# Performance work log

Measured on AMD Instinct MI355X. Metric: run time of the kernel, lower is better.

## Reference

```python
import jax, jax.numpy as jnp
import numpy as np

N, E, IN, H, ED = 50000, 800000, 128, 128, 3
EPS = 1e-5

def _gat_conv(x, src, dst, ea, W, a_src, a_dst, We, a_edge, bias):
    n = x.shape[0]
    # add self loops; self-loop edge_attr = per-feature mean (PyG fill_value='mean')
    loops = jnp.arange(n, dtype=src.dtype)
    s = jnp.concatenate([src, loops])
    d = jnp.concatenate([dst, loops])
    ea_full = jnp.concatenate([ea, jnp.broadcast_to(ea.mean(0), (n, ea.shape[1]))], 0)
    h = x @ W                       # [n, H]
    al_s = h @ a_src                # [n]
    al_d = h @ a_dst
    al_e = (ea_full @ We) @ a_edge  # [E+n]
    alpha = jax.nn.leaky_relu(al_s[s] + al_d[d] + al_e, 0.2)
    # segment softmax over destination nodes (every node has a self loop)
    amax = jax.ops.segment_max(alpha, d, num_segments=n)
    ex = jnp.exp(alpha - amax[d])
    denom = jax.ops.segment_sum(ex, d, num_segments=n)
    coef = ex / (denom[d] + 1e-16)
    out = jax.ops.segment_sum(h[s] * coef[:, None], d, num_segments=n)
    return out + bias

def _bn(x, gamma, beta):
    mu = x.mean(0)
    var = ((x - mu) ** 2).mean(0)
    return (x - mu) * jax.lax.rsqrt(var + EPS) * gamma + beta

def setup_inputs():
    key = jax.random.key(0)
    ks = jax.random.split(key, 40)
    inp = {
        "x": jax.random.normal(ks[0], (N, IN), jnp.float32),
        "edge_index": jax.random.randint(ks[1], (2, E), 0, N, dtype=jnp.int32),
        "batch": jnp.zeros((N,), jnp.int32),
        "edge_attr": jax.random.normal(ks[2], (E, ED), jnp.float32),
    }
    i = 3
    for l, cin in ((1, IN), (2, H), (3, H)):
        s = 1.0 / np.sqrt(cin)
        inp[f"W{l}"] = jax.random.normal(ks[i], (cin, H), jnp.float32) * s; i += 1
        inp[f"as{l}"] = jax.random.normal(ks[i], (H,), jnp.float32) * 0.1; i += 1
        inp[f"ad{l}"] = jax.random.normal(ks[i], (H,), jnp.float32) * 0.1; i += 1
        inp[f"We{l}"] = jax.random.normal(ks[i], (ED, H), jnp.float32) * 0.5; i += 1
        inp[f"ae{l}"] = jax.random.normal(ks[i], (H,), jnp.float32) * 0.1; i += 1
        inp[f"b{l}"] = jnp.zeros((H,), jnp.float32)
        inp[f"g{l}"] = jnp.ones((H,), jnp.float32)
        inp[f"be{l}"] = jnp.zeros((H,), jnp.float32)
    return inp

def reference(x, edge_index, batch, edge_attr,
              W1, as1, ad1, We1, ae1, b1, g1, be1,
              W2, as2, ad2, We2, ae2, b2, g2, be2,
              W3, as3, ad3, We3, ae3, b3, g3, be3):
    src, dst = edge_index[0], edge_index[1]
    h = _gat_conv(x, src, dst, edge_attr, W1, as1, ad1, We1, ae1, b1)
    h = _bn(jax.nn.leaky_relu(h, 0.01), g1, be1)
    h = _gat_conv(h, src, dst, edge_attr, W2, as2, ad2, We2, ae2, b2)
    h = _bn(jax.nn.leaky_relu(h, 0.01), g2, be2)
    h = _gat_conv(h, src, dst, edge_attr, W3, as3, ad3, We3, ae3, b3)
    h = _bn(jax.nn.leaky_relu(h, 0.01), g3, be3)
    return h
```

## Files before the change

### kernel.cpp

```cpp
#include <hip/hip_runtime.h>
#include <math.h>


struct __align__(16) Edge { int src; float e0, e1, e2; };

__global__ void k_hist(const int* __restrict__ dst, int E, int* __restrict__ deg) {
  int i = blockIdx.x * blockDim.x + threadIdx.x;
  if (i < E) atomicAdd(&deg[dst[i]], 1);
}

__global__ void k_ea_sum(const float* __restrict__ ea, int E, float* __restrict__ ea_sum) {
  float s0 = 0.f, s1 = 0.f, s2 = 0.f;
  for (int i = blockIdx.x * blockDim.x + threadIdx.x; i < E; i += gridDim.x * blockDim.x) {
    s0 += ea[i * 3 + 0]; s1 += ea[i * 3 + 1]; s2 += ea[i * 3 + 2];
  }
  for (int off = 32; off; off >>= 1) {
    s0 += __shfl_down(s0, off); s1 += __shfl_down(s1, off); s2 += __shfl_down(s2, off);
  }
  __shared__ float ls[3][4];
  int lane = threadIdx.x & 63, w = threadIdx.x >> 6;
  if (lane == 0) { ls[0][w] = s0; ls[1][w] = s1; ls[2][w] = s2; }
  __syncthreads();
  if (threadIdx.x == 0) {
    float t0 = 0.f, t1 = 0.f, t2 = 0.f;
    for (int ww = 0; ww < 4; ++ww) { t0 += ls[0][ww]; t1 += ls[1][ww]; t2 += ls[2][ww]; }
    atomicAdd(&ea_sum[0], t0); atomicAdd(&ea_sum[1], t1); atomicAdd(&ea_sum[2], t2);
  }
}

__device__ __forceinline__ int wave_incl_scan(int x, int lane) {
  for (int off = 1; off < 64; off <<= 1) {
    int t = __shfl_up(x, off);
    if (lane >= off) x += t;
  }
  return x;
}

__global__ __launch_bounds__(1024) void k_scan_a(const int* __restrict__ deg, int n,
                                                 int* __restrict__ start,
                                                 int* __restrict__ bsum) {
  __shared__ int wsum[16];
  int t = threadIdx.x, lane = t & 63, w = t >> 6;
  int i = blockIdx.x * 1024 + t;
  int v = (i < n) ? deg[i] : 0;
  int x = wave_incl_scan(v, lane);
  if (lane == 63) wsum[w] = x;
  __syncthreads();
  if (w == 0 && lane < 16) {
    int s = wsum[lane];
    for (int off = 1; off < 16; off <<= 1) {
      int u = __shfl_up(s, off);
      if (lane >= off) s += u;
    }
    wsum[lane] = s;
  }
  __syncthreads();
  int woff = w ? wsum[w - 1] : 0;
  if (i < n) start[i] = x - v + woff;
  if (t == 1023) bsum[blockIdx.x] = wsum[15];
}

__global__ void k_scan_b(int* __restrict__ bsum, int nb, int* __restrict__ start, int n) {
  int lane = threadIdx.x;
  int v = (lane < nb) ? bsum[lane] : 0;
  int x = wave_incl_scan(v, lane);
  if (lane < nb) bsum[lane] = x - v;
  if (lane == nb - 1) start[n] = x;
}

__global__ void k_scan_c(int* __restrict__ start, const int* __restrict__ bsum, int n,
                         int* __restrict__ cursor) {
  int i = blockIdx.x * blockDim.x + threadIdx.x;
  if (i < n) {
    int s = start[i] + bsum[i >> 10];
    start[i] = s;
    cursor[i] = s;
  }
}

__global__ void k_scatter(const int* __restrict__ src, const int* __restrict__ dst,
                          const float* __restrict__ ea, int E,
                          int* __restrict__ cursor, Edge* __restrict__ edges,
                          int* __restrict__ srcs, int* __restrict__ dsts) {
  int i = blockIdx.x * blockDim.x + threadIdx.x;
  if (i >= E) return;
  int d = dst[i];
  int pos = atomicAdd(&cursor[d], 1);
  Edge e;
  int s = src[i];
  e.src = s;
  e.e0 = ea[i * 3 + 0]; e.e1 = ea[i * 3 + 1]; e.e2 = ea[i * 3 + 2];
  edges[pos] = e;
  srcs[pos] = s;
  dsts[pos] = d;
}

__global__ void k_initid(float* __restrict__ sc, float* __restrict__ sh) {
  int c = threadIdx.x;
  sc[c] = 1.f; sh[c] = 0.f;
}

__global__ void k_param(const float* __restrict__ We, const float* __restrict__ ae,
                        const float* __restrict__ ea_sum, float invE, float* __restrict__ P) {
  int lane = threadIdx.x;
  float a0 = ae[lane], a1 = ae[64 + lane];
  float p0 = We[0 * 128 + lane] * a0 + We[0 * 128 + 64 + lane] * a1;
  float p1 = We[1 * 128 + lane] * a0 + We[1 * 128 + 64 + lane] * a1;
  float p2 = We[2 * 128 + lane] * a0 + We[2 * 128 + 64 + lane] * a1;
  for (int off = 32; off; off >>= 1) {
    p0 += __shfl_down(p0, off); p1 += __shfl_down(p1, off); p2 += __shfl_down(p2, off);
  }
  if (lane == 0) {
    P[0] = p0; P[1] = p1; P[2] = p2;
    P[3] = ea_sum[0] * invE * p0 + ea_sum[1] * invE * p1 + ea_sum[2] * invE * p2;
  }
}

__global__ __launch_bounds__(256) void k_gemm2(
    const float* __restrict__ X, const float* __restrict__ Wm,
    const float* __restrict__ bnsc, const float* __restrict__ bnsh,
    const float* __restrict__ as, const float* __restrict__ ad,
    const float* __restrict__ P,
    float* __restrict__ h, float* __restrict__ al_s, float* __restrict__ al_d,
    float* __restrict__ es, int n) {
  __shared__ float wl[128 * 128];
  __shared__ float xs[32 * 128];
  int t = threadIdx.x;
  for (int i = t; i < 4096; i += 256) ((float4*)wl)[i] = ((const float4*)Wm)[i];
  int c32 = t & 31;
  int c4 = c32 << 2;
  int rq = t >> 5;
  int lane = t & 63;
  float4 av_s = *(const float4*)(as + c4);
  float4 av_d = *(const float4*)(ad + c4);
  float cself = P[3];
  int ntiles = (n + 31) >> 5;
  for (int tile = blockIdx.x; tile < ntiles; tile += gridDim.x) {
    int r0 = tile << 5;
    __syncthreads();
    for (int i = t; i < 1024; i += 256) {
      int rr = i >> 5, cc = i & 31;
      int g = r0 + rr;
      float4 v;
      if (g < n) {
        v = ((const float4*)(X + (size_t)g * 128))[cc];
        float4 sc = ((const float4*)bnsc)[cc];
        float4 sh = ((const float4*)bnsh)[cc];
        v.x = fmaf(v.x, sc.x, sh.x); v.y = fmaf(v.y, sc.y, sh.y);
        v.z = fmaf(v.z, sc.z, sh.z); v.w = fmaf(v.w, sc.w, sh.w);
      } else { v.x = v.y = v.z = v.w = 0.f; }
      ((float4*)xs)[i] = v;
    }
    __syncthreads();
    float4 acc[4];
    for (int r = 0; r < 4; ++r) { acc[r].x = acc[r].y = acc[r].z = acc[r].w = 0.f; }
    const float* xr = xs + (rq << 2) * 128;
#pragma unroll 4
    for (int k = 0; k < 128; ++k) {
      float4 w4 = ((const float4*)wl)[(k << 5) + c32];
#pragma unroll
      for (int r = 0; r < 4; ++r) {
        float xv = xr[r * 128 + k];
        acc[r].x = fmaf(xv, w4.x, acc[r].x);
        acc[r].y = fmaf(xv, w4.y, acc[r].y);
        acc[r].z = fmaf(xv, w4.z, acc[r].z);
        acc[r].w = fmaf(xv, w4.w, acc[r].w);
      }
    }
    int gbase = r0 + (rq << 2);
#pragma unroll
    for (int r = 0; r < 4; ++r) {
      int g = gbase + r;
      float4 o = acc[r];
      if (g < n) *(float4*)(h + (size_t)g * 128 + c4) = o;
      float ps = o.x * av_s.x + o.y * av_s.y + o.z * av_s.z + o.w * av_s.w;
      float pd = o.x * av_d.x + o.y * av_d.y + o.z * av_d.z + o.w * av_d.w;
      for (int off = 16; off; off >>= 1) {
        ps += __shfl_xor(ps, off);
        pd += __shfl_xor(pd, off);
      }
      if ((lane & 31) == 0 && g < n) {
        al_s[g] = ps; al_d[g] = pd;
        float a = ps + pd + cself;
        a = a > 0.f ? a : 0.2f * a;
        es[g] = __expf(a);
      }
    }
  }
}

__global__ __launch_bounds__(256) void k_alpha2(const float4* __restrict__ edges,
                                                const int* __restrict__ dsts,
                                                const float* __restrict__ al_s,
                                                const float* __restrict__ al_d,
                                                const float* __restrict__ P,
                                                float* __restrict__ pexp, int E) {
  int i = blockIdx.x * blockDim.x + threadIdx.x;
  if (i >= E) return;
  float4 ef = edges[i];
  int s = __float_as_int(ef.x);
  float a = al_s[s] + al_d[dsts[i]] + ef.y * P[0] + ef.z * P[1] + ef.w * P[2];
  a = a > 0.f ? a : 0.2f * a;
  pexp[i] = __expf(a);
}

__global__ __launch_bounds__(256) void k_agg3(const int* __restrict__ srcs,
                                              const float* __restrict__ pexp,
                                              const int* __restrict__ start,
                                              const float* __restrict__ h,
                                              const float* __restrict__ es,
                                              const float* __restrict__ bias,
                                              float* __restrict__ y,
                                              float* __restrict__ colsum,
                                              float* __restrict__ colsumsq, int n) {
  int lane = threadIdx.x & 63;
  int w = threadIdx.x >> 6;
  int gw = (blockIdx.x * blockDim.x + threadIdx.x) >> 6;
  int nw = (gridDim.x * blockDim.x) >> 6;
  float2 b2 = ((const float2*)bias)[lane];
  float s0 = 0.f, s1 = 0.f, q0 = 0.f, q1 = 0.f;
  for (int i = gw; i < n; i += nw) {
    int e0 = start[i];
    int deg = start[i + 1] - e0;
    float eself = es[i];
    float2 h2 = ((const float2*)(h + (size_t)i * 128))[lane];
    float accA0 = eself * h2.x, accA1 = eself * h2.y;
    float accB0 = 0.f, accB1 = 0.f, accC0 = 0.f, accC1 = 0.f, accD0 = 0.f, accD1 = 0.f;
    float pacc = 0.f;
    for (int base = 0; base < deg; base += 64) {
      int j = base + lane;
      float p = 0.f; int sidx = 0;
      if (j < deg) { p = pexp[e0 + j]; sidx = srcs[e0 + j]; }
      pacc += p;
      int cnt = deg - base; if (cnt > 64) cnt = 64;
      int tt = 0;
      for (; tt + 4 <= cnt; tt += 4) {
        float pa = __shfl(p, tt),     pb = __shfl(p, tt + 1);
        float pc = __shfl(p, tt + 2), pd = __shfl(p, tt + 3);
        int sa = __shfl(sidx, tt),     sb = __shfl(sidx, tt + 1);
        int sc = __shfl(sidx, tt + 2), sd = __shfl(sidx, tt + 3);
        float2 ha = ((const float2*)(h + (size_t)sa * 128))[lane];
        float2 hb = ((const float2*)(h + (size_t)sb * 128))[lane];
        float2 hc = ((const float2*)(h + (size_t)sc * 128))[lane];
        float2 hd = ((const float2*)(h + (size_t)sd * 128))[lane];
        accA0 = fmaf(pa, ha.x, accA0); accA1 = fmaf(pa, ha.y, accA1);
        accB0 = fmaf(pb, hb.x, accB0); accB1 = fmaf(pb, hb.y, accB1);
        accC0 = fmaf(pc, hc.x, accC0); accC1 = fmaf(pc, hc.y, accC1);
        accD0 = fmaf(pd, hd.x, accD0); accD1 = fmaf(pd, hd.y, accD1);
      }
      for (; tt < cnt; ++tt) {
        float pa = __shfl(p, tt); int sa = __shfl(sidx, tt);
        float2 ha = ((const float2*)(h + (size_t)sa * 128))[lane];
        accA0 = fmaf(pa, ha.x, accA0); accA1 = fmaf(pa, ha.y, accA1);
      }
    }
    for (int off = 32; off; off >>= 1) pacc += __shfl_xor(pacc, off);
    float inv = 1.0f / (eself + pacc + 1e-16f);
    float o0 = (accA0 + accB0) + (accC0 + accD0);
    float o1 = (accA1 + accB1) + (accC1 + accD1);
    o0 = fmaf(o0, inv, b2.x);
    o1 = fmaf(o1, inv, b2.y);
    o0 = o0 > 0.f ? o0 : 0.01f * o0;
    o1 = o1 > 0.f ? o1 : 0.01f * o1;
    float2 o2 = {o0, o1};
    ((float2*)(y + (size_t)i * 128))[lane] = o2;
    s0 += o0; s1 += o1;
    q0 = fmaf(o0, o0, q0); q1 = fmaf(o1, o1, q1);
  }
  __shared__ float red[4][4][64];
  red[0][w][lane] = s0; red[1][w][lane] = s1; red[2][w][lane] = q0; red[3][w][lane] = q1;
  __syncthreads();
  if (w == 0) {
    for (int ww = 1; ww < 4; ++ww) {
      s0 += red[0][ww][lane]; s1 += red[1][ww][lane];
      q0 += red[2][ww][lane]; q1 += red[3][ww][lane];
    }
    atomicAdd(&colsum[2 * lane], s0);
    atomicAdd(&colsum[2 * lane + 1], s1);
    atomicAdd(&colsumsq[2 * lane], q0);
    atomicAdd(&colsumsq[2 * lane + 1], q1);
  }
}

__global__ void k_bnfinal(const float* __restrict__ colsum, const float* __restrict__ colsumsq,
                          const float* __restrict__ g, const float* __restrict__ be,
                          float invN, float* __restrict__ scale, float* __restrict__ shift) {
  int c = threadIdx.x;
  float mu = colsum[c] * invN;
  float var = colsumsq[c] * invN - mu * mu;
  var = var > 0.f ? var : 0.f;
  float sc = g[c] * rsqrtf(var + 1e-5f);
  scale[c] = sc;
  shift[c] = be[c] - mu * sc;
}

__global__ void k_bnapply(const float4* __restrict__ yin, const float* __restrict__ scale,
                          const float* __restrict__ shift, float4* __restrict__ yout, int total4) {
  int i = blockIdx.x * blockDim.x + threadIdx.x;
  if (i >= total4) return;
  int c4 = i & 31;
  float4 v = yin[i];
  float4 sc = ((const float4*)scale)[c4];
  float4 sh = ((const float4*)shift)[c4];
  v.x = fmaf(v.x, sc.x, sh.x);
  v.y = fmaf(v.y, sc.y, sh.y);
  v.z = fmaf(v.z, sc.z, sh.z);
  v.w = fmaf(v.w, sc.w, sh.w);
  yout[i] = v;
}

extern "C" void kernel_launch(void* const* d_in, const int* in_sizes, int n_in,
                              void* d_out, int out_size, void* d_ws, size_t ws_size,
                              hipStream_t stream) {
  const float* x = (const float*)d_in[0];
  const int* eidx = (const int*)d_in[1];
  const float* ea = (const float*)d_in[3];
  const int H = 128;
  const int N = in_sizes[0] / H;
  const int E = in_sizes[1] / 2;
  const int* srcIdx = eidx;
  const int* dstIdx = eidx + E;

  char* ws = (char*)d_ws;
  size_t off = 0;
  auto alloc = [&](size_t bytes) -> void* {
    void* p = ws + off;
    off = (off + bytes + 255) & ~(size_t)255;
    return p;
  };
  Edge* edges = (Edge*)alloc((size_t)E * sizeof(Edge));
  int* srcs = (int*)alloc((size_t)E * sizeof(int));
  int* dsts = (int*)alloc((size_t)E * sizeof(int));
  float* pexp = (float*)alloc((size_t)E * sizeof(float));
  float* h = (float*)alloc((size_t)N * H * sizeof(float));
  float* y = (float*)alloc((size_t)N * H * sizeof(float));
  float* al_s = (float*)alloc((size_t)N * sizeof(float));
  float* al_d = (float*)alloc((size_t)N * sizeof(float));
  float* es = (float*)alloc((size_t)N * sizeof(float));
  int* deg = (int*)alloc((size_t)N * sizeof(int));
  int* start = (int*)alloc((size_t)(N + 1) * sizeof(int));
  int* cursor = (int*)alloc((size_t)N * sizeof(int));
  int* bsum = (int*)alloc(64 * sizeof(int));
  float* colsum = (float*)alloc(128 * sizeof(float));
  float* colsumsq = (float*)alloc(128 * sizeof(float));
  float* scale = (float*)alloc(128 * sizeof(float));
  float* shift = (float*)alloc(128 * sizeof(float));
  float* ea_sum = (float*)alloc(16 * sizeof(float));
  float* P = (float*)alloc(16 * sizeof(float));

  const int nb = (N + 1023) / 1024;

  hipMemsetAsync(deg, 0, (size_t)N * sizeof(int), stream);
  hipMemsetAsync(ea_sum, 0, 16 * sizeof(float), stream);
  k_hist<<<(E + 255) / 256, 256, 0, stream>>>(dstIdx, E, deg);
  k_ea_sum<<<256, 256, 0, stream>>>(ea, E, ea_sum);
  k_scan_a<<<nb, 1024, 0, stream>>>(deg, N, start, bsum);
  k_scan_b<<<1, 64, 0, stream>>>(bsum, nb, start, N);
  k_scan_c<<<(N + 255) / 256, 256, 0, stream>>>(start, bsum, N, cursor);
  k_scatter<<<(E + 255) / 256, 256, 0, stream>>>(srcIdx, dstIdx, ea, E, cursor, edges, srcs, dsts);
  k_initid<<<1, 128, 0, stream>>>(scale, shift);

  const float* X = x;
  for (int l = 0; l < 3; ++l) {
    const float* W = (const float*)d_in[4 + 8 * l + 0];
    const float* as = (const float*)d_in[4 + 8 * l + 1];
    const float* ad = (const float*)d_in[4 + 8 * l + 2];
    const float* We = (const float*)d_in[4 + 8 * l + 3];
    const float* ae = (const float*)d_in[4 + 8 * l + 4];
    const float* b = (const float*)d_in[4 + 8 * l + 5];
    const float* g = (const float*)d_in[4 + 8 * l + 6];
    const float* be = (const float*)d_in[4 + 8 * l + 7];

    hipMemsetAsync(colsum, 0, 128 * sizeof(float), stream);
    hipMemsetAsync(colsumsq, 0, 128 * sizeof(float), stream);
    k_param<<<1, 64, 0, stream>>>(We, ae, ea_sum, 1.0f / (float)E, P);
    k_gemm2<<<512, 256, 0, stream>>>(X, W, scale, shift, as, ad, P, h, al_s, al_d, es, N);
    k_alpha2<<<(E + 255) / 256, 256, 0, stream>>>((const float4*)edges, dsts, al_s, al_d, P,
                                                  pexp, E);
    k_agg3<<<2048, 256, 0, stream>>>(srcs, pexp, start, h, es, b, y, colsum, colsumsq, N);
    k_bnfinal<<<1, 128, 0, stream>>>(colsum, colsumsq, g, be, 1.0f / (float)N, scale, shift);
    X = y;
  }
  k_bnapply<<<((N * 32) + 255) / 256, 256, 0, stream>>>((const float4*)y, scale, shift,
                                                        (float4*)d_out, N * 32);
}
```

Before: 850.2 us.

## Store node features as bf16 and gather with scalar-indexed unrolled loop

The GEMM now writes the projected node features h as packed bf16 pairs instead of fp32, which halves the bytes moved by the random per-edge gathers in aggregation. The aggregation kernel also stops loading edges cooperatively and shuffling them. It reads src and pexp with wave-uniform addresses, using readfirstlane bounds, and issues 8 independent gathers per iteration to keep more memory requests in flight. The cost is lower precision in the aggregated features, which risks tolerance failures across three layers.

```diff
diff --git a/kernel.cpp b/kernel.cpp
--- a/kernel.cpp
+++ b/kernel.cpp
@@ -3,6 +3,12 @@
 
 
 struct __align__(16) Edge { int src; float e0, e1, e2; };
+
+__device__ __forceinline__ unsigned short f2bf(float x) {
+  unsigned u = __float_as_uint(x);
+  unsigned r = (u + 0x7FFFu + ((u >> 16) & 1u)) >> 16;
+  return (unsigned short)r;
+}
 
 __global__ void k_hist(const int* __restrict__ dst, int E, int* __restrict__ deg) {
   int i = blockIdx.x * blockDim.x + threadIdx.x;
@@ -121,7 +127,7 @@
     const float* __restrict__ bnsc, const float* __restrict__ bnsh,
     const float* __restrict__ as, const float* __restrict__ ad,
     const float* __restrict__ P,
-    float* __restrict__ h, float* __restrict__ al_s, float* __restrict__ al_d,
+    unsigned* __restrict__ hb, float* __restrict__ al_s, float* __restrict__ al_d,
     float* __restrict__ es, int n) {
   __shared__ float wl[128 * 128];
   __shared__ float xs[32 * 128];
@@ -172,7 +178,12 @@
     for (int r = 0; r < 4; ++r) {
       int g = gbase + r;
       float4 o = acc[r];
-      if (g < n) *(float4*)(h + (size_t)g * 128 + c4) = o;
+      if (g < n) {
+        unsigned u01 = ((unsigned)f2bf(o.y) << 16) | (unsigned)f2bf(o.x);
+        unsigned u23 = ((unsigned)f2bf(o.w) << 16) | (unsigned)f2bf(o.z);
+        uint2 uu = {u01, u23};
+        *(uint2*)(hb + (size_t)g * 64 + (c32 << 1)) = uu;
+      }
       float ps = o.x * av_s.x + o.y * av_s.y + o.z * av_s.z + o.w * av_s.w;
       float pd = o.x * av_d.x + o.y * av_d.y + o.z * av_d.z + o.w * av_d.w;
       for (int off = 16; off; off >>= 1) {
@@ -204,10 +215,10 @@
   pexp[i] = __expf(a);
 }
 
-__global__ __launch_bounds__(256) void k_agg3(const int* __restrict__ srcs,
+__global__ __launch_bounds__(256) void k_agg4(const int* __restrict__ srcs,
                                               const float* __restrict__ pexp,
                                               const int* __restrict__ start,
-                                              const float* __restrict__ h,
+                                              const unsigned* __restrict__ hb,
                                               const float* __restrict__ es,
                                               const float* __restrict__ bias,
                                               float* __restrict__ y,
@@ -220,44 +231,47 @@
   float2 b2 = ((const float2*)bias)[lane];
   float s0 = 0.f, s1 = 0.f, q0 = 0.f, q1 = 0.f;
   for (int i = gw; i < n; i += nw) {
-    int e0 = start[i];
-    int deg = start[i + 1] - e0;
+    int e0 = __builtin_amdgcn_readfirstlane(start[i]);
+    int e1 = __builtin_amdgcn_readfirstlane(start[i + 1]);
     float eself = es[i];
-    float2 h2 = ((const float2*)(h + (size_t)i * 128))[lane];
-    float accA0 = eself * h2.x, accA1 = eself * h2.y;
-    float accB0 = 0.f, accB1 = 0.f, accC0 = 0.f, accC1 = 0.f, accD0 = 0.f, accD1 = 0.f;
+    unsigned hv = hb[(size_t)i * 64 + lane];
+    float hx = __uint_as_float(hv << 16);
+    float hy = __uint_as_float(hv & 0xFFFF0000u);
+    float aX0 = eself * hx, aY0 = eself * hy;
+    float aX1 = 0.f, aY1 = 0.f, aX2 = 0.f, aY2 = 0.f, aX3 = 0.f, aY3 = 0.f;
     float pacc = 0.f;
-    for (int base = 0; base < deg; base += 64) {
-      int j = base + lane;
-      float p = 0.f; int sidx = 0;
-      if (j < deg) { p = pexp[e0 + j]; sidx = srcs[e0 + j]; }
-      pacc += p;
-      int cnt = deg - base; if (cnt > 64) cnt = 64;
-      int tt = 0;
-      for (; tt + 4 <= cnt; tt += 4) {
-        float pa = __shfl(p, tt),     pb = __shfl(p, tt + 1);
-        float pc = __shfl(p, tt + 2), pd = __shfl(p, tt + 3);
-        int sa = __shfl(sidx, tt),     sb = __shfl(sidx, tt + 1);
-        int sc = __shfl(sidx, tt + 2), sd = __shfl(sidx, tt + 3);
-        float2 ha = ((const float2*)(h + (size_t)sa * 128))[lane];
-        float2 hb = ((const float2*)(h + (size_t)sb * 128))[lane];
-        float2 hc = ((const float2*)(h + (size_t)sc * 128))[lane];
-        float2 hd = ((const float2*)(h + (size_t)sd * 128))[lane];
-        accA0 = fmaf(pa, ha.x, accA0); accA1 = fmaf(pa, ha.y, accA1);
-        accB0 = fmaf(pb, hb.x, accB0); accB1 = fmaf(pb, hb.y, accB1);
-        accC0 = fmaf(pc, hc.x, accC0); accC1 = fmaf(pc, hc.y, accC1);
-        accD0 = fmaf(pd, hd.x, accD0); accD1 = fmaf(pd, hd.y, accD1);
+    int e = e0;
+    for (; e + 8 <= e1; e += 8) {
+      int sv[8]; float pv[8]; unsigned gv[8];
+#pragma unroll
+      for (int k = 0; k < 8; ++k) sv[k] = srcs[e + k];
+#pragma unroll
+      for (int k = 0; k < 8; ++k) pv[k] = pexp[e + k];
+#pragma unroll
+      for (int k = 0; k < 8; ++k) gv[k] = hb[(size_t)sv[k] * 64 + lane];
+#pragma unroll
+      for (int k = 0; k < 8; ++k) {
+        float gx = __uint_as_float(gv[k] << 16);
+        float gy = __uint_as_float(gv[k] & 0xFFFF0000u);
+        pacc += pv[k];
+        if ((k & 3) == 0) { aX0 = fmaf(pv[k], gx, aX0); aY0 = fmaf(pv[k], gy, aY0); }
+        else if ((k & 3) == 1) { aX1 = fmaf(pv[k], gx, aX1); aY1 = fmaf(pv[k], gy, aY1); }
+        else if ((k & 3) == 2) { aX2 = fmaf(pv[k], gx, aX2); aY2 = fmaf(pv[k], gy, aY2); }
+        else { aX3 = fmaf(pv[k], gx, aX3); aY3 = fmaf(pv[k], gy, aY3); }
       }
-      for (; tt < cnt; ++tt) {
-        float pa = __shfl(p, tt); int sa = __shfl(sidx, tt);
-        float2 ha = ((const float2*)(h + (size_t)sa * 128))[lane];
-        accA0 = fmaf(pa, ha.x, accA0); accA1 = fmaf(pa, ha.y, accA1);
-      }
-    }
-    for (int off = 32; off; off >>= 1) pacc += __shfl_xor(pacc, off);
+    }
+    for (; e < e1; ++e) {
+      int sv = srcs[e];
+      float pv = pexp[e];
+      unsigned gv = hb[(size_t)sv * 64 + lane];
+      float gx = __uint_as_float(gv << 16);
+      float gy = __uint_as_float(gv & 0xFFFF0000u);
+      pacc += pv;
+      aX0 = fmaf(pv, gx, aX0); aY0 = fmaf(pv, gy, aY0);
+    }
     float inv = 1.0f / (eself + pacc + 1e-16f);
-    float o0 = (accA0 + accB0) + (accC0 + accD0);
-    float o1 = (accA1 + accB1) + (accC1 + accD1);
+    float o0 = (aX0 + aX1) + (aX2 + aX3);
+    float o1 = (aY0 + aY1) + (aY2 + aY3);
     o0 = fmaf(o0, inv, b2.x);
     o1 = fmaf(o1, inv, b2.y);
     o0 = o0 > 0.f ? o0 : 0.01f * o0;
@@ -332,7 +346,7 @@
   int* srcs = (int*)alloc((size_t)E * sizeof(int));
   int* dsts = (int*)alloc((size_t)E * sizeof(int));
   float* pexp = (float*)alloc((size_t)E * sizeof(float));
-  float* h = (float*)alloc((size_t)N * H * sizeof(float));
+  unsigned* hb = (unsigned*)alloc((size_t)N * 64 * sizeof(unsigned));
   float* y = (float*)alloc((size_t)N * H * sizeof(float));
   float* al_s = (float*)alloc((size_t)N * sizeof(float));
   float* al_d = (float*)alloc((size_t)N * sizeof(float));
@@ -374,10 +388,10 @@
     hipMemsetAsync(colsum, 0, 128 * sizeof(float), stream);
     hipMemsetAsync(colsumsq, 0, 128 * sizeof(float), stream);
     k_param<<<1, 64, 0, stream>>>(We, ae, ea_sum, 1.0f / (float)E, P);
-    k_gemm2<<<512, 256, 0, stream>>>(X, W, scale, shift, as, ad, P, h, al_s, al_d, es, N);
+    k_gemm2<<<512, 256, 0, stream>>>(X, W, scale, shift, as, ad, P, hb, al_s, al_d, es, N);
     k_alpha2<<<(E + 255) / 256, 256, 0, stream>>>((const float4*)edges, dsts, al_s, al_d, P,
                                                   pexp, E);
-    k_agg3<<<2048, 256, 0, stream>>>(srcs, pexp, start, h, es, b, y, colsum, colsumsq, N);
+    k_agg4<<<2048, 256, 0, stream>>>(srcs, pexp, start, hb, es, b, y, colsum, colsumsq, N);
     k_bnfinal<<<1, 128, 0, stream>>>(colsum, colsumsq, g, be, 1.0f / (float)N, scale, shift);
     X = y;
   }
```

New measurement: 783.4 us. 7.9% less time.
